# Kernel optimization log

Hardware: AMD Instinct MI355X
Metric: run time of the kernel (lower is better)

The kernel has to match this reference:

```python
import jax, jax.numpy as jnp
import numpy as np

HIDDEN = 2048
NUM_HEADS = 32
NUM_KV_HEADS = 8
HEAD_DIM = HIDDEN // NUM_HEADS  # 64
GROUP = NUM_HEADS // NUM_KV_HEADS  # 4
B, S = 2, 2048


def setup_inputs() -> dict:
    key = jax.random.key(0)
    ks = jax.random.split(key, 9)
    sc = 0.02
    kv_dim = NUM_KV_HEADS * HEAD_DIM
    return {
        "x": jax.random.normal(ks[0], (B, S, HIDDEN), jnp.float32),
        # weights stored as [in, out] (transpose of torch Linear.weight)
        "Wq": jax.random.normal(ks[1], (HIDDEN, HIDDEN), jnp.float32) * sc,
        "bq": jnp.zeros((HIDDEN,), jnp.float32),
        "Wk": jax.random.normal(ks[2], (HIDDEN, kv_dim), jnp.float32) * sc,
        "bk": jnp.zeros((kv_dim,), jnp.float32),
        "Wv": jax.random.normal(ks[3], (HIDDEN, kv_dim), jnp.float32) * sc,
        "bv": jnp.zeros((kv_dim,), jnp.float32),
        "Wo": jax.random.normal(ks[4], (HIDDEN, HIDDEN), jnp.float32) * sc,
        "bo": jnp.zeros((HIDDEN,), jnp.float32),
    }


def reference(x, Wq, bq, Wk, bk, Wv, bv, Wo, bo):
    b, s, _ = x.shape
    q = (x @ Wq + bq).reshape(b, s, NUM_KV_HEADS, GROUP, HEAD_DIM)
    k = (x @ Wk + bk).reshape(b, s, NUM_KV_HEADS, HEAD_DIM)
    v = (x @ Wv + bv).reshape(b, s, NUM_KV_HEADS, HEAD_DIM)
    scale = 1.0 / jnp.sqrt(jnp.asarray(HEAD_DIM, x.dtype))
    # scores: [b, g(kv heads), r(q per group), s(query), t(key)]
    scores = jnp.einsum("bsgrd,btgd->bgrst", q, k) * scale
    attn = jax.nn.softmax(scores, axis=-1)  # dropout rate 0 -> identity
    out = jnp.einsum("bgrst,btgd->bsgrd", attn, v).reshape(b, s, HIDDEN)
    return out @ Wo + bo
```

## Files before the change

kernel.cpp:

```cpp
#include <hip/hip_runtime.h>

#define HIDDEN 2048
#define NHEADS 32
#define NKV 8
#define HD 64
#define BATCH 2
#define SEQ 2048
#define KVD 512
#define BSZ 4096
#define QKVD 3072

typedef __bf16 bfx8 __attribute__((ext_vector_type(8)));
typedef __bf16 bfx4 __attribute__((ext_vector_type(4)));
typedef float f32x4 __attribute__((ext_vector_type(4)));

#define QSCALE 0.1803368801111204f

__device__ __forceinline__ int swP(int row, int k) {
    return row * 64 + (k ^ ((row & 7) << 3) ^ ((row & 8) << 1));
}

__device__ __forceinline__ void gl_lds16(const __bf16* g, __bf16* l) {
    __builtin_amdgcn_global_load_lds(
        (const __attribute__((address_space(1))) unsigned int*)g,
        (__attribute__((address_space(3))) unsigned int*)l, 16, 0, 0);
}

__global__ __launch_bounds__(256) void cvt_bf16(const float* __restrict__ src,
                                                __bf16* __restrict__ dst, int n4) {
    int i = blockIdx.x * 256 + threadIdx.x;
    if (i >= n4) return;
    float4 f = ((const float4*)src)[i];
    bfx4 o = {(__bf16)f.x, (__bf16)f.y, (__bf16)f.z, (__bf16)f.w};
    *(bfx4*)(dst + (size_t)i * 4) = o;
}

__device__ __forceinline__ void tcvt_tile(const float* __restrict__ src,
                                          __bf16* __restrict__ dst,
                                          int R, int C, int tx, int ty,
                                          float (*tile)[65], int t, float mul) {
    int br = ty * 64, bc = tx * 64;
    {
        int r = t >> 4, c = (t & 15) * 4;
#pragma unroll
        for (int i = 0; i < 4; ++i) {
            float4 v = *(const float4*)(&src[(long)(br + r + i * 16) * C + bc + c]);
            tile[r + i * 16][c + 0] = v.x * mul;
            tile[r + i * 16][c + 1] = v.y * mul;
            tile[r + i * 16][c + 2] = v.z * mul;
            tile[r + i * 16][c + 3] = v.w * mul;
        }
    }
    __syncthreads();
    {
        int d = t >> 2, tt0 = (t & 3) * 16;
        bfx8 o0, o1;
#pragma unroll
        for (int j = 0; j < 8; ++j) o0[j] = (__bf16)tile[tt0 + j][d];
#pragma unroll
        for (int j = 0; j < 8; ++j) o1[j] = (__bf16)tile[tt0 + 8 + j][d];
        *(bfx8*)(&dst[(long)(bc + d) * R + br + tt0]) = o0;
        *(bfx8*)(&dst[(long)(bc + d) * R + br + tt0 + 8]) = o1;
    }
}

__global__ __launch_bounds__(256) void prep(const float* __restrict__ Wq,
                                            const float* __restrict__ Wk,
                                            const float* __restrict__ Wv,
                                            const float* __restrict__ Wo,
                                            const float* __restrict__ bq,
                                            const float* __restrict__ bk,
                                            const float* __restrict__ bv,
                                            __bf16* __restrict__ wqkvt,
                                            __bf16* __restrict__ wot,
                                            float* __restrict__ bqkv) {
    __shared__ float tile[64][65];
    int idx = blockIdx.x, t = threadIdx.x;
    if (idx < 1024) {
        tcvt_tile(Wq, wqkvt, HIDDEN, HIDDEN, idx & 31, idx >> 5, tile, t, QSCALE);
    } else if (idx < 1280) {
        int l = idx - 1024;
        tcvt_tile(Wk, wqkvt + (size_t)HIDDEN * HIDDEN, HIDDEN, KVD, l & 7, l >> 3, tile, t, 1.0f);
    } else if (idx < 1536) {
        int l = idx - 1280;
        tcvt_tile(Wv, wqkvt + (size_t)(HIDDEN + KVD) * HIDDEN, HIDDEN, KVD, l & 7, l >> 3, tile, t, 1.0f);
    } else if (idx < 2560) {
        int l = idx - 1536;
        tcvt_tile(Wo, wot, HIDDEN, HIDDEN, l & 31, l >> 5, tile, t, 1.0f);
    } else {
        int i = (idx - 2560) * 256 + t;
        if (i < QKVD) {
            float v = (i < HIDDEN) ? bq[i] * QSCALE
                                   : (i < HIDDEN + KVD ? bk[i - HIDDEN] : bv[i - HIDDEN - KVD]);
            bqkv[i] = v;
        }
    }
}

__global__ __launch_bounds__(256) void transpose_v(const __bf16* __restrict__ qkv,
                                                   __bf16* __restrict__ vt) {
    __shared__ __bf16 tile[64][65];
    int t = threadIdx.x;
    int nb0 = blockIdx.x * 64;
    int bh = blockIdx.y;
    int b = bh >> 3, kv = bh & 7;
    {
        int tt = t >> 2, c0 = (t & 3) * 16;
        const __bf16* p = &qkv[(long)(b * SEQ + nb0 + tt) * QKVD + HIDDEN + KVD + kv * HD + c0];
        bfx8 a0 = *(const bfx8*)(p);
        bfx8 a1 = *(const bfx8*)(p + 8);
#pragma unroll
        for (int j = 0; j < 8; ++j) tile[tt][c0 + j] = a0[j];
#pragma unroll
        for (int j = 0; j < 8; ++j) tile[tt][c0 + 8 + j] = a1[j];
    }
    __syncthreads();
    {
        int d = t >> 2, tt0 = (t & 3) * 16;
        bfx8 o0, o1;
#pragma unroll
        for (int j = 0; j < 8; ++j) o0[j] = tile[tt0 + j][d];
#pragma unroll
        for (int j = 0; j < 8; ++j) o1[j] = tile[tt0 + 8 + j][d];
        __bf16* q = &vt[((long)bh * HD + d) * SEQ + nb0 + tt0];
        *(bfx8*)(q) = o0;
        *(bfx8*)(q + 8) = o1;
    }
}

template <bool OUT_BF16>
__global__ __launch_bounds__(256, 3) void gemm128(const __bf16* __restrict__ A,
                                                  const __bf16* __restrict__ Bt,
                                                  const float* __restrict__ bias,
                                                  void* __restrict__ C,
                                                  int M, int N, int K) {
    __shared__ __align__(16) __bf16 As[2][128 * 32];
    __shared__ __align__(16) __bf16 Bs[2][128 * 32];
    int t = threadIdx.x;
    int w = t >> 6, lane = t & 63;
    int lrow = lane & 15, quad = lane >> 4;
    long m0 = (long)blockIdx.y * 128, n0 = (long)blockIdx.x * 128;
    int wr = (w >> 1) * 64, wc = (w & 1) * 64;
    f32x4 acc[4][4] = {};
    int srow = t >> 2, scol = (t & 3) * 8;
    const __bf16* Ag = A + (m0 + srow) * (long)K + scol;
    const __bf16* Bg = Bt + (n0 + srow) * (long)K + scol;
#define STAGE_G(kb, buf)                                                      \
    {                                                                         \
        _Pragma("unroll") for (int c = 0; c < 2; ++c) {                       \
            gl_lds16(Ag + (long)c * 64 * K + (kb), &As[buf][c * 2048 + w * 512]); \
            gl_lds16(Bg + (long)c * 64 * K + (kb), &Bs[buf][c * 2048 + w * 512]); \
        }                                                                     \
    }
    STAGE_G(0, 0);
    int nk = K >> 5;
    for (int it = 0; it < nk; ++it) {
        __syncthreads();
        if (it + 1 < nk) STAGE_G((it + 1) * 32, (it + 1) & 1);
        const __bf16* Ab = &As[it & 1][0];
        const __bf16* Bb = &Bs[it & 1][0];
        bfx8 af[4], bfr[4];
#pragma unroll
        for (int i = 0; i < 4; ++i) af[i] = *(const bfx8*)&Ab[(wr + i * 16 + lrow) * 32 + quad * 8];
#pragma unroll
        for (int j = 0; j < 4; ++j) bfr[j] = *(const bfx8*)&Bb[(wc + j * 16 + lrow) * 32 + quad * 8];
#pragma unroll
        for (int i = 0; i < 4; ++i)
#pragma unroll
            for (int j = 0; j < 4; ++j)
                acc[i][j] = __builtin_amdgcn_mfma_f32_16x16x32_bf16(af[i], bfr[j], acc[i][j], 0, 0, 0);
    }
#undef STAGE_G
#pragma unroll
    for (int j = 0; j < 4; ++j) {
        long col = n0 + wc + j * 16 + lrow;
        float bv = bias[col];
#pragma unroll
        for (int i = 0; i < 4; ++i) {
#pragma unroll
            for (int r = 0; r < 4; ++r) {
                long row = m0 + wr + i * 16 + quad * 4 + r;
                float val = acc[i][j][r] + bv;
                if (OUT_BF16)
                    ((__bf16*)C)[row * N + col] = (__bf16)val;
                else
                    ((float*)C)[row * N + col] = val;
            }
        }
    }
}

__global__ __launch_bounds__(256, 2) void attn(const __bf16* __restrict__ QKV,
                                               const __bf16* __restrict__ Vt,
                                               __bf16* __restrict__ O) {
    __shared__ __align__(16) __bf16 Ks[2][64 * 64];
    __shared__ __align__(16) __bf16 Vs[2][64 * 64];
    __shared__ __align__(16) __bf16 Ps[4][64 * 64];
    int t = threadIdx.x;
    int w = t >> 6, lane = t & 63;
    int lrow = lane & 15, quad = lane >> 4;
    int qb = blockIdx.x, bh = blockIdx.y;
    int b = bh >> 5, h = bh & 31, kv = h >> 2;
    int q0 = qb * 256 + w * 64;

    bfx8 qf[4][2];
#pragma unroll
    for (int i = 0; i < 4; ++i)
#pragma unroll
        for (int kk = 0; kk < 2; ++kk)
            qf[i][kk] = *(const bfx8*)(QKV + (long)(b * SEQ + q0 + i * 16 + lrow) * QKVD +
                                       h * HD + kk * 32 + quad * 8);

    int srow = t >> 2, scol = (t & 3) * 8;
    const __bf16* kg = QKV + (long)(b * SEQ + srow) * QKVD + HIDDEN + kv * HD + scol;
    const __bf16* vg = Vt + ((long)(b * NKV + kv) * HD + srow) * SEQ + scol;
#define STAGE_KV(nb, buf)                                                          \
    {                                                                              \
        _Pragma("unroll") for (int c = 0; c < 2; ++c) {                            \
            gl_lds16(kg + (long)(nb)*QKVD + c * 32, &Ks[buf][c * 2048 + w * 512]); \
            gl_lds16(vg + (nb) + c * 32, &Vs[buf][c * 2048 + w * 512]);            \
        }                                                                          \
    }
    STAGE_KV(0, 0);

    f32x4 accO[4][4] = {};
    f32x4 lacc[4] = {};
    bfx8 ones;
#pragma unroll
    for (int j = 0; j < 8; ++j) ones[j] = (__bf16)1.0f;
    __bf16* myPs = &Ps[w][0];

    for (int it = 0; it < SEQ / 64; ++it) {
        __syncthreads();
        if (it + 1 < SEQ / 64) STAGE_KV((it + 1) * 64, (it + 1) & 1);
        const __bf16* Kb = &Ks[it & 1][0];
        const __bf16* Vb = &Vs[it & 1][0];
        bfx8 kb[2][4];
#pragma unroll
        for (int kk = 0; kk < 2; ++kk)
#pragma unroll
            for (int c = 0; c < 4; ++c)
                kb[kk][c] = *(const bfx8*)&Kb[kk * 2048 + c * 512 + lrow * 32 + quad * 8];
#pragma unroll
        for (int i = 0; i < 4; ++i) {
            f32x4 s[4] = {};
#pragma unroll
            for (int kk = 0; kk < 2; ++kk)
#pragma unroll
                for (int c = 0; c < 4; ++c)
                    s[c] = __builtin_amdgcn_mfma_f32_16x16x32_bf16(qf[i][kk], kb[kk][c], s[c], 0, 0, 0);
#pragma unroll
            for (int c = 0; c < 4; ++c)
#pragma unroll
                for (int r = 0; r < 4; ++r) {
                    float p = __builtin_amdgcn_exp2f(s[c][r]);
                    myPs[swP(i * 16 + quad * 4 + r, c * 16 + lrow)] = (__bf16)p;
                }
        }
#pragma unroll
        for (int kk = 0; kk < 2; ++kk) {
            bfx8 pa[4];
#pragma unroll
            for (int i = 0; i < 4; ++i)
                pa[i] = *(const bfx8*)&myPs[swP(i * 16 + lrow, kk * 32 + quad * 8)];
#pragma unroll
            for (int c = 0; c < 4; ++c) {
                bfx8 vb = *(const bfx8*)&Vb[kk * 2048 + c * 512 + lrow * 32 + quad * 8];
#pragma unroll
                for (int i = 0; i < 4; ++i)
                    accO[i][c] = __builtin_amdgcn_mfma_f32_16x16x32_bf16(pa[i], vb, accO[i][c], 0, 0, 0);
            }
#pragma unroll
            for (int i = 0; i < 4; ++i)
                lacc[i] = __builtin_amdgcn_mfma_f32_16x16x32_bf16(pa[i], ones, lacc[i], 0, 0, 0);
        }
    }
#pragma unroll
    for (int i = 0; i < 4; ++i) {
        f32x4 inv;
#pragma unroll
        for (int r = 0; r < 4; ++r) inv[r] = 1.0f / lacc[i][r];
#pragma unroll
        for (int c = 0; c < 4; ++c)
#pragma unroll
            for (int r = 0; r < 4; ++r) {
                long row = (long)(b * SEQ + q0 + i * 16 + quad * 4 + r);
                O[row * HIDDEN + h * HD + c * 16 + lrow] = (__bf16)(accO[i][c][r] * inv[r]);
            }
    }
#undef STAGE_KV
}

extern "C" void kernel_launch(void* const* d_in, const int* in_sizes, int n_in,
                              void* d_out, int out_size, void* d_ws, size_t ws_size,
                              hipStream_t stream) {
    const float* x  = (const float*)d_in[0];
    const float* Wq = (const float*)d_in[1];
    const float* bq = (const float*)d_in[2];
    const float* Wk = (const float*)d_in[3];
    const float* bk = (const float*)d_in[4];
    const float* Wv = (const float*)d_in[5];
    const float* bv = (const float*)d_in[6];
    const float* Wo = (const float*)d_in[7];
    const float* bo = (const float*)d_in[8];
    float* out = (float*)d_out;

    __bf16* ws    = (__bf16*)d_ws;
    __bf16* xb    = ws;
    __bf16* wqkvt = xb + (size_t)BSZ * HIDDEN;
    __bf16* wot   = wqkvt + (size_t)QKVD * HIDDEN;
    __bf16* qkv   = wot + (size_t)HIDDEN * HIDDEN;
    __bf16* vt_   = qkv + (size_t)BSZ * QKVD;
    __bf16* ab_   = vt_ + (size_t)BSZ * KVD;
    float*  bqkv  = (float*)(ab_ + (size_t)BSZ * HIDDEN);

    cvt_bf16<<<(BSZ * HIDDEN / 4 + 255) / 256, 256, 0, stream>>>(x, xb, BSZ * HIDDEN / 4);
    prep<<<2560 + (QKVD + 255) / 256, 256, 0, stream>>>(Wq, Wk, Wv, Wo, bq, bk, bv,
                                                        wqkvt, wot, bqkv);

    gemm128<true><<<dim3(QKVD / 128, BSZ / 128), 256, 0, stream>>>(xb, wqkvt, bqkv, qkv, BSZ, QKVD, HIDDEN);

    transpose_v<<<dim3(SEQ / 64, BATCH * NKV), 256, 0, stream>>>(qkv, vt_);
    attn<<<dim3(SEQ / 256, BATCH * NHEADS), 256, 0, stream>>>(qkv, vt_, ab_);

    gemm128<false><<<dim3(HIDDEN / 128, BSZ / 128), 256, 0, stream>>>(ab_, wot, bo, out, BSZ, HIDDEN, HIDDEN);
}
```

Before: 325.8 us.

## Keep attention probabilities in registers via transposed S and swizzle LDS tiles

```diff
diff --git a/kernel.cpp b/kernel.cpp
--- a/kernel.cpp
+++ b/kernel.cpp
@@ -13,12 +13,17 @@
 typedef __bf16 bfx8 __attribute__((ext_vector_type(8)));
 typedef __bf16 bfx4 __attribute__((ext_vector_type(4)));
 typedef float f32x4 __attribute__((ext_vector_type(4)));
+typedef short sx4v __attribute__((ext_vector_type(4)));
 
 #define QSCALE 0.1803368801111204f
 
-__device__ __forceinline__ int swP(int row, int k) {
-    return row * 64 + (k ^ ((row & 7) << 3) ^ ((row & 8) << 1));
-}
+#if defined(__AMDGCN__) && __has_builtin(__builtin_amdgcn_mfma_f32_16x16x16_bf16)
+#define MFMA16(a, b, c) __builtin_amdgcn_mfma_f32_16x16x16_bf16(a, b, c, 0, 0, 0)
+#else
+#define MFMA16(a, b, c)                                                    \
+    __builtin_amdgcn_mfma_f32_16x16x16bf16_1k(__builtin_bit_cast(sx4v, (a)), \
+                                              __builtin_bit_cast(sx4v, (b)), (c), 0, 0, 0)
+#endif
 
 __device__ __forceinline__ void gl_lds16(const __bf16* g, __bf16* l) {
     __builtin_amdgcn_global_load_lds(
@@ -142,7 +147,8 @@
     long m0 = (long)blockIdx.y * 128, n0 = (long)blockIdx.x * 128;
     int wr = (w >> 1) * 64, wc = (w & 1) * 64;
     f32x4 acc[4][4] = {};
-    int srow = t >> 2, scol = (t & 3) * 8;
+    int srow = t >> 2, scol = (((t & 3) ^ ((t >> 3) & 3))) * 8;
+    int sA = (lrow >> 1) & 3;
     const __bf16* Ag = A + (m0 + srow) * (long)K + scol;
     const __bf16* Bg = Bt + (n0 + srow) * (long)K + scol;
 #define STAGE_G(kb, buf)                                                      \
@@ -161,9 +167,11 @@
         const __bf16* Bb = &Bs[it & 1][0];
         bfx8 af[4], bfr[4];
 #pragma unroll
-        for (int i = 0; i < 4; ++i) af[i] = *(const bfx8*)&Ab[(wr + i * 16 + lrow) * 32 + quad * 8];
-#pragma unroll
-        for (int j = 0; j < 4; ++j) bfr[j] = *(const bfx8*)&Bb[(wc + j * 16 + lrow) * 32 + quad * 8];
+        for (int i = 0; i < 4; ++i)
+            af[i] = *(const bfx8*)&Ab[(wr + i * 16 + lrow) * 32 + ((quad ^ sA) * 8)];
+#pragma unroll
+        for (int j = 0; j < 4; ++j)
+            bfr[j] = *(const bfx8*)&Bb[(wc + j * 16 + lrow) * 32 + ((quad ^ sA) * 8)];
 #pragma unroll
         for (int i = 0; i < 4; ++i)
 #pragma unroll
@@ -195,7 +203,6 @@
                                                __bf16* __restrict__ O) {
     __shared__ __align__(16) __bf16 Ks[2][64 * 64];
     __shared__ __align__(16) __bf16 Vs[2][64 * 64];
-    __shared__ __align__(16) __bf16 Ps[4][64 * 64];
     int t = threadIdx.x;
     int w = t >> 6, lane = t & 63;
     int lrow = lane & 15, quad = lane >> 4;
@@ -211,7 +218,8 @@
             qf[i][kk] = *(const bfx8*)(QKV + (long)(b * SEQ + q0 + i * 16 + lrow) * QKVD +
                                        h * HD + kk * 32 + quad * 8);
 
-    int srow = t >> 2, scol = (t & 3) * 8;
+    int srow = t >> 2, scol = (((t & 3) ^ ((t >> 3) & 3))) * 8;
+    int sA = (lrow >> 1) & 3;
     const __bf16* kg = QKV + (long)(b * SEQ + srow) * QKVD + HIDDEN + kv * HD + scol;
     const __bf16* vg = Vt + ((long)(b * NKV + kv) * HD + srow) * SEQ + scol;
 #define STAGE_KV(nb, buf)                                                          \
@@ -224,69 +232,63 @@
     STAGE_KV(0, 0);
 
     f32x4 accO[4][4] = {};
-    f32x4 lacc[4] = {};
-    bfx8 ones;
-#pragma unroll
-    for (int j = 0; j < 8; ++j) ones[j] = (__bf16)1.0f;
-    __bf16* myPs = &Ps[w][0];
+    float lacc[4] = {0.f, 0.f, 0.f, 0.f};
 
     for (int it = 0; it < SEQ / 64; ++it) {
         __syncthreads();
         if (it + 1 < SEQ / 64) STAGE_KV((it + 1) * 64, (it + 1) & 1);
         const __bf16* Kb = &Ks[it & 1][0];
         const __bf16* Vb = &Vs[it & 1][0];
-        bfx8 kb[2][4];
-#pragma unroll
-        for (int kk = 0; kk < 2; ++kk)
-#pragma unroll
-            for (int c = 0; c < 4; ++c)
-                kb[kk][c] = *(const bfx8*)&Kb[kk * 2048 + c * 512 + lrow * 32 + quad * 8];
-#pragma unroll
-        for (int i = 0; i < 4; ++i) {
-            f32x4 s[4] = {};
-#pragma unroll
-            for (int kk = 0; kk < 2; ++kk)
-#pragma unroll
-                for (int c = 0; c < 4; ++c)
-                    s[c] = __builtin_amdgcn_mfma_f32_16x16x32_bf16(qf[i][kk], kb[kk][c], s[c], 0, 0, 0);
-#pragma unroll
-            for (int c = 0; c < 4; ++c)
-#pragma unroll
-                for (int r = 0; r < 4; ++r) {
-                    float p = __builtin_amdgcn_exp2f(s[c][r]);
-                    myPs[swP(i * 16 + quad * 4 + r, c * 16 + lrow)] = (__bf16)p;
-                }
-        }
-#pragma unroll
-        for (int kk = 0; kk < 2; ++kk) {
-            bfx8 pa[4];
-#pragma unroll
-            for (int i = 0; i < 4; ++i)
-                pa[i] = *(const bfx8*)&myPs[swP(i * 16 + lrow, kk * 32 + quad * 8)];
-#pragma unroll
-            for (int c = 0; c < 4; ++c) {
-                bfx8 vb = *(const bfx8*)&Vb[kk * 2048 + c * 512 + lrow * 32 + quad * 8];
+#pragma unroll
+        for (int tt = 0; tt < 4; ++tt) {
+            bfx8 ka0 = *(const bfx8*)&Kb[tt * 512 + lrow * 32 + ((quad ^ sA) * 8)];
+            bfx8 ka1 = *(const bfx8*)&Kb[2048 + tt * 512 + lrow * 32 + ((quad ^ sA) * 8)];
+            f32x4 s2[4];
+#pragma unroll
+            for (int i = 0; i < 4; ++i) {
+                f32x4 z = {};
+                z = __builtin_amdgcn_mfma_f32_16x16x32_bf16(ka0, qf[i][0], z, 0, 0, 0);
+                s2[i] = __builtin_amdgcn_mfma_f32_16x16x32_bf16(ka1, qf[i][1], z, 0, 0, 0);
+            }
+            bfx4 pb[4];
+#pragma unroll
+            for (int i = 0; i < 4; ++i) {
+                float p0 = __builtin_amdgcn_exp2f(s2[i][0]);
+                float p1 = __builtin_amdgcn_exp2f(s2[i][1]);
+                float p2 = __builtin_amdgcn_exp2f(s2[i][2]);
+                float p3 = __builtin_amdgcn_exp2f(s2[i][3]);
+                lacc[i] += (p0 + p1) + (p2 + p3);
+                bfx4 pp = {(__bf16)p0, (__bf16)p1, (__bf16)p2, (__bf16)p3};
+                pb[i] = pp;
+            }
+            int vbase = (tt >> 1) * 2048 + lrow * 32 +
+                        ((((tt & 1) * 2 + (quad >> 1)) ^ sA) * 8) + (quad & 1) * 4;
+#pragma unroll
+            for (int dt = 0; dt < 4; ++dt) {
+                bfx4 va = *(const bfx4*)&Vb[vbase + dt * 512];
 #pragma unroll
                 for (int i = 0; i < 4; ++i)
-                    accO[i][c] = __builtin_amdgcn_mfma_f32_16x16x32_bf16(pa[i], vb, accO[i][c], 0, 0, 0);
+                    accO[dt][i] = MFMA16(va, pb[i], accO[dt][i]);
             }
-#pragma unroll
-            for (int i = 0; i < 4; ++i)
-                lacc[i] = __builtin_amdgcn_mfma_f32_16x16x32_bf16(pa[i], ones, lacc[i], 0, 0, 0);
-        }
-    }
+        }
+    }
+    float inv[4];
 #pragma unroll
     for (int i = 0; i < 4; ++i) {
-        f32x4 inv;
-#pragma unroll
-        for (int r = 0; r < 4; ++r) inv[r] = 1.0f / lacc[i][r];
-#pragma unroll
-        for (int c = 0; c < 4; ++c)
-#pragma unroll
-            for (int r = 0; r < 4; ++r) {
-                long row = (long)(b * SEQ + q0 + i * 16 + quad * 4 + r);
-                O[row * HIDDEN + h * HD + c * 16 + lrow] = (__bf16)(accO[i][c][r] * inv[r]);
-            }
+        float l = lacc[i];
+        l += __shfl_xor(l, 16);
+        l += __shfl_xor(l, 32);
+        inv[i] = 1.0f / l;
+    }
+#pragma unroll
+    for (int i = 0; i < 4; ++i) {
+        long row = (long)(b * SEQ + q0 + i * 16 + lrow);
+#pragma unroll
+        for (int dt = 0; dt < 4; ++dt) {
+            bfx4 o4 = {(__bf16)(accO[dt][i][0] * inv[i]), (__bf16)(accO[dt][i][1] * inv[i]),
+                       (__bf16)(accO[dt][i][2] * inv[i]), (__bf16)(accO[dt][i][3] * inv[i])};
+            *(bfx4*)&O[row * HIDDEN + h * HD + dt * 16 + quad * 4] = o4;
+        }
     }
 #undef STAGE_KV
 }
```

Result: no change. 320.0 us (-1.8%).
